# Kernel tuning notes

Hardware: AMD Instinct MI355X
Metric: run time of the kernel (lower is better)

The kernel has to match this reference:

```python
import jax, jax.numpy as jnp
import numpy as np

N = 8192
NFEAT = 512
NHID = 256
NCLASS = 40
EDGE_P = 0.002  # ~16 avg degree


def setup_inputs() -> dict:
    key = jax.random.key(0)
    k1, k2, k3, k4 = jax.random.split(key, 4)
    x = jax.random.normal(k1, (N, NFEAT), dtype=jnp.float32)
    # unnormalized binary adjacency without self loops (module adds eye itself)
    adj = (jax.random.uniform(k2, (N, N)) < EDGE_P).astype(jnp.float32)
    # GCNConv weights: torch.rand(in, out) -> uniform[0,1)
    W1 = jax.random.uniform(k3, (NFEAT, NHID), dtype=jnp.float32)
    W2 = jax.random.uniform(k4, (NHID, NCLASS), dtype=jnp.float32)
    return {"x": x, "adj": adj, "W1": W1, "W2": W2}


def reference(x, adj, W1, W2):
    n = adj.shape[0]
    # add self loops: in_adj.to_dense() + eye
    A_hat = adj + jnp.eye(n, dtype=adj.dtype)
    # normalize_adj: D^{-1/2} A_hat D^{-1/2} (diag matmuls == row/col scaling)
    d = A_hat.sum(-1) ** -0.5  # [N]
    norm_adj = d[:, None] * A_hat * d[None, :]
    # conv1: relu(adj @ x @ W1); dropout is identity in eval mode
    h = jax.nn.relu((norm_adj @ x) @ W1)
    # conv2 reuses the same normalized adjacency (only one DGG layer by default)
    h2 = jax.nn.relu((norm_adj @ h) @ W2)
    return jax.nn.log_softmax(h2, axis=-1)
```

## Files before the change

kernel.cpp:

```cpp
#include <hip/hip_runtime.h>
#include <math.h>

#define NV 8192
#define CAP 64

typedef __attribute__((ext_vector_type(8))) short short8;
typedef __attribute__((ext_vector_type(4))) float f32x4;

static __device__ __forceinline__ unsigned short f2bf(float v) {
  unsigned int u = __float_as_uint(v);
  unsigned int r = (u + 0x7fffu + ((u >> 16) & 1u)) >> 16;
  return (unsigned short)r;
}
static __device__ __forceinline__ float bf2f(unsigned short h) {
  return __uint_as_float(((unsigned int)h) << 16);
}

__global__ __launch_bounds__(256) void build_graph(
    const float* __restrict__ adj, int* __restrict__ cols,
    int* __restrict__ rowcount, float* __restrict__ dinv,
    float* __restrict__ diagv) {
  int row = blockIdx.x;
  int t = threadIdx.x;
  int lane = t & 63;
  __shared__ int cnt;
  __shared__ int diag_nz;
  __shared__ int wsum[4];
  if (t == 0) { cnt = 0; diag_nz = 0; }
  __syncthreads();
  const float4* arow = (const float4*)(adj + (size_t)row * NV);
  int mycount = 0;
  for (int i = t; i < NV / 4; i += 256) {
    float4 v = arow[i];
    float va[4] = {v.x, v.y, v.z, v.w};
#pragma unroll
    for (int j = 0; j < 4; j++) {
      bool nz = (va[j] != 0.0f);
      mycount += nz ? 1 : 0;
      int c = i * 4 + j;
      bool isdiag = nz && (c == row);
      bool take = nz && !isdiag;
      if (isdiag) diag_nz = 1;
      unsigned long long m = __ballot(take);
      if (m != 0ull) {
        int tot = __popcll(m);
        int pre = __popcll(m & ((1ull << lane) - 1ull));
        int leader = __ffsll((unsigned long long)m) - 1;
        int base = 0;
        if (lane == leader) base = atomicAdd(&cnt, tot);
        base = __shfl(base, leader, 64);
        if (take) {
          int p = base + pre;
          if (p < CAP) cols[(size_t)row * CAP + p] = c;
        }
      }
    }
  }
  for (int off = 32; off > 0; off >>= 1) mycount += __shfl_xor(mycount, off, 64);
  if (lane == 0) wsum[t >> 6] = mycount;
  __syncthreads();
  if (t == 0) {
    int nnz = wsum[0] + wsum[1] + wsum[2] + wsum[3];
    float deg = (float)nnz + 1.0f;
    dinv[row] = 1.0f / sqrtf(deg);
    diagv[row] = diag_nz ? 2.0f : 1.0f;
    rowcount[row] = cnt > CAP ? CAP : cnt;
  }
}

__global__ __launch_bounds__(256) void split_a(
    const float* __restrict__ x, unsigned short* __restrict__ Ah,
    unsigned short* __restrict__ Al) {
  int i = blockIdx.x * 256 + threadIdx.x;
  float4 v = ((const float4*)x)[i];
  ushort4 h, l;
  h.x = f2bf(v.x); l.x = f2bf(v.x - bf2f(h.x));
  h.y = f2bf(v.y); l.y = f2bf(v.y - bf2f(h.y));
  h.z = f2bf(v.z); l.z = f2bf(v.z - bf2f(h.z));
  h.w = f2bf(v.w); l.w = f2bf(v.w - bf2f(h.w));
  ((ushort4*)Ah)[i] = h;
  ((ushort4*)Al)[i] = l;
}

__global__ __launch_bounds__(256) void split_w1t(
    const float* __restrict__ W1, unsigned short* __restrict__ Bh,
    unsigned short* __restrict__ Bl) {
  int n = blockIdx.x;
  int k = blockIdx.y * 256 + threadIdx.x;
  float v = W1[(size_t)k * 256 + n];
  unsigned short h = f2bf(v);
  Bh[(size_t)n * 512 + k] = h;
  Bl[(size_t)n * 512 + k] = f2bf(v - bf2f(h));
}

__global__ __launch_bounds__(256) void gemm1_mfma(
    const unsigned short* __restrict__ Ah, const unsigned short* __restrict__ Al,
    const unsigned short* __restrict__ Bh, const unsigned short* __restrict__ Bl,
    float* __restrict__ C) {
  const int K = 512;
  __shared__ __align__(16) unsigned short sAh[128][40];
  __shared__ __align__(16) unsigned short sAl[128][40];
  __shared__ __align__(16) unsigned short sBh[64][40];
  __shared__ __align__(16) unsigned short sBl[64][40];
  int t = threadIdx.x;
  int bn = blockIdx.x * 64;
  int bm = blockIdx.y * 128;
  int lane = t & 63, w = t >> 6;
  int quad = lane >> 4, m16 = lane & 15;
  f32x4 acc[2][4] = {};
  for (int k0 = 0; k0 < K; k0 += 32) {
#pragma unroll
    for (int i = 0; i < 2; i++) {
      int id = t + i * 256;
      int row = id >> 2, q = id & 3;
      *(uint4*)&sAh[row][q * 8] = *(const uint4*)&Ah[(size_t)(bm + row) * K + k0 + q * 8];
      *(uint4*)&sAl[row][q * 8] = *(const uint4*)&Al[(size_t)(bm + row) * K + k0 + q * 8];
    }
    {
      int row = t >> 2, q = t & 3;
      *(uint4*)&sBh[row][q * 8] = *(const uint4*)&Bh[(size_t)(bn + row) * K + k0 + q * 8];
      *(uint4*)&sBl[row][q * 8] = *(const uint4*)&Bl[(size_t)(bn + row) * K + k0 + q * 8];
    }
    __syncthreads();
    short8 ah[2], al[2], bh[4], bl[4];
#pragma unroll
    for (int i = 0; i < 2; i++) {
      ah[i] = *(const short8*)&sAh[w * 32 + i * 16 + m16][quad * 8];
      al[i] = *(const short8*)&sAl[w * 32 + i * 16 + m16][quad * 8];
    }
#pragma unroll
    for (int j = 0; j < 4; j++) {
      bh[j] = *(const short8*)&sBh[j * 16 + m16][quad * 8];
      bl[j] = *(const short8*)&sBl[j * 16 + m16][quad * 8];
    }
#pragma unroll
    for (int i = 0; i < 2; i++)
#pragma unroll
      for (int j = 0; j < 4; j++) {
        acc[i][j] = __builtin_amdgcn_mfma_f32_16x16x32_bf16(ah[i], bh[j], acc[i][j], 0, 0, 0);
        acc[i][j] = __builtin_amdgcn_mfma_f32_16x16x32_bf16(al[i], bh[j], acc[i][j], 0, 0, 0);
        acc[i][j] = __builtin_amdgcn_mfma_f32_16x16x32_bf16(ah[i], bl[j], acc[i][j], 0, 0, 0);
      }
    __syncthreads();
  }
#pragma unroll
  for (int i = 0; i < 2; i++)
#pragma unroll
    for (int j = 0; j < 4; j++)
#pragma unroll
      for (int r = 0; r < 4; r++)
        C[(size_t)(bm + w * 32 + i * 16 + quad * 4 + r) * 256 + bn + j * 16 + m16] =
            acc[i][j][r];
}

__global__ __launch_bounds__(256) void gemm_f32(
    const float* __restrict__ A, const float* __restrict__ B,
    float* __restrict__ C, int M, int K, int Nvalid, int ldb, int ldc) {
  __shared__ float As[16][68];
  __shared__ float Bs[16][64];
  int t = threadIdx.x;
  int bm0 = blockIdx.y * 64;
  int bn0 = blockIdx.x * 64;
  int tx = t & 15, ty = t >> 4;
  int ar = t >> 2;
  int ak = (t & 3) * 4;
  int bk = t >> 4;
  int bn = (t & 15) * 4;
  float acc[4][4] = {};
  for (int k0 = 0; k0 < K; k0 += 16) {
    float4 av = *(const float4*)(A + (size_t)(bm0 + ar) * K + k0 + ak);
    float4 bv;
    int bc = bn0 + bn;
    if (bc + 3 < Nvalid) {
      bv = *(const float4*)(B + (size_t)(k0 + bk) * ldb + bc);
    } else {
      bv.x = (bc + 0 < Nvalid) ? B[(size_t)(k0 + bk) * ldb + bc + 0] : 0.0f;
      bv.y = (bc + 1 < Nvalid) ? B[(size_t)(k0 + bk) * ldb + bc + 1] : 0.0f;
      bv.z = (bc + 2 < Nvalid) ? B[(size_t)(k0 + bk) * ldb + bc + 2] : 0.0f;
      bv.w = (bc + 3 < Nvalid) ? B[(size_t)(k0 + bk) * ldb + bc + 3] : 0.0f;
    }
    As[ak + 0][ar] = av.x;
    As[ak + 1][ar] = av.y;
    As[ak + 2][ar] = av.z;
    As[ak + 3][ar] = av.w;
    *(float4*)(&Bs[bk][bn]) = bv;
    __syncthreads();
#pragma unroll
    for (int kk = 0; kk < 16; kk++) {
      float4 a = *(const float4*)(&As[kk][ty * 4]);
      float4 b = *(const float4*)(&Bs[kk][tx * 4]);
      acc[0][0] += a.x * b.x; acc[0][1] += a.x * b.y; acc[0][2] += a.x * b.z; acc[0][3] += a.x * b.w;
      acc[1][0] += a.y * b.x; acc[1][1] += a.y * b.y; acc[1][2] += a.y * b.z; acc[1][3] += a.y * b.w;
      acc[2][0] += a.z * b.x; acc[2][1] += a.z * b.y; acc[2][2] += a.z * b.z; acc[2][3] += a.z * b.w;
      acc[3][0] += a.w * b.x; acc[3][1] += a.w * b.y; acc[3][2] += a.w * b.z; acc[3][3] += a.w * b.w;
    }
    __syncthreads();
  }
#pragma unroll
  for (int i = 0; i < 4; i++) {
    *(float4*)(C + (size_t)(bm0 + ty * 4 + i) * ldc + bn0 + tx * 4) =
        make_float4(acc[i][0], acc[i][1], acc[i][2], acc[i][3]);
  }
}

__global__ __launch_bounds__(256) void spmm_relu_k(
    const float* __restrict__ Z, const int* __restrict__ cols,
    const int* __restrict__ rowcount, const float* __restrict__ dinv,
    const float* __restrict__ diagv, float* __restrict__ H) {
  int lane = threadIdx.x & 63;
  int row = blockIdx.x * 4 + (threadIdx.x >> 6);
  const float4* Zr = (const float4*)Z;
  float di = dinv[row];
  float4 z = Zr[(size_t)row * 64 + lane];
  float dd = diagv[row] * di;
  float4 acc;
  acc.x = dd * z.x; acc.y = dd * z.y; acc.z = dd * z.z; acc.w = dd * z.w;
  int cnt = rowcount[row];
  const int* cr = cols + (size_t)row * CAP;
  int e = 0;
  for (; e + 4 <= cnt; e += 4) {
    int c0 = cr[e + 0], c1 = cr[e + 1], c2 = cr[e + 2], c3 = cr[e + 3];
    float w0 = dinv[c0], w1 = dinv[c1], w2 = dinv[c2], w3 = dinv[c3];
    float4 g0 = Zr[(size_t)c0 * 64 + lane];
    float4 g1 = Zr[(size_t)c1 * 64 + lane];
    float4 g2 = Zr[(size_t)c2 * 64 + lane];
    float4 g3 = Zr[(size_t)c3 * 64 + lane];
    acc.x += w0 * g0.x + w1 * g1.x + w2 * g2.x + w3 * g3.x;
    acc.y += w0 * g0.y + w1 * g1.y + w2 * g2.y + w3 * g3.y;
    acc.z += w0 * g0.z + w1 * g1.z + w2 * g2.z + w3 * g3.z;
    acc.w += w0 * g0.w + w1 * g1.w + w2 * g2.w + w3 * g3.w;
  }
  for (; e < cnt; e++) {
    int c = cr[e];
    float w = dinv[c];
    float4 g = Zr[(size_t)c * 64 + lane];
    acc.x += w * g.x; acc.y += w * g.y; acc.z += w * g.z; acc.w += w * g.w;
  }
  float4 o;
  o.x = fmaxf(acc.x * di, 0.0f);
  o.y = fmaxf(acc.y * di, 0.0f);
  o.z = fmaxf(acc.z * di, 0.0f);
  o.w = fmaxf(acc.w * di, 0.0f);
  ((float4*)H)[(size_t)row * 64 + lane] = o;
}

__global__ __launch_bounds__(256) void spmm2_lsm_k(
    const float* __restrict__ Z, const int* __restrict__ cols,
    const int* __restrict__ rowcount, const float* __restrict__ dinv,
    const float* __restrict__ diagv, float* __restrict__ out) {
  int lane = threadIdx.x & 63;
  int row = blockIdx.x * 4 + (threadIdx.x >> 6);
  float di = dinv[row];
  float acc = diagv[row] * di * Z[(size_t)row * 64 + lane];
  int cnt = rowcount[row];
  const int* cr = cols + (size_t)row * CAP;
  int e = 0;
  for (; e + 4 <= cnt; e += 4) {
    int c0 = cr[e + 0], c1 = cr[e + 1], c2 = cr[e + 2], c3 = cr[e + 3];
    float w0 = dinv[c0], w1 = dinv[c1], w2 = dinv[c2], w3 = dinv[c3];
    acc += w0 * Z[(size_t)c0 * 64 + lane] + w1 * Z[(size_t)c1 * 64 + lane] +
           w2 * Z[(size_t)c2 * 64 + lane] + w3 * Z[(size_t)c3 * 64 + lane];
  }
  for (; e < cnt; e++) {
    int c = cr[e];
    acc += dinv[c] * Z[(size_t)c * 64 + lane];
  }
  float h2 = (lane < 40) ? fmaxf(acc * di, 0.0f) : -INFINITY;
  float m = h2;
  for (int off = 32; off > 0; off >>= 1) m = fmaxf(m, __shfl_xor(m, off, 64));
  float ex = (lane < 40) ? expf(h2 - m) : 0.0f;
  float s = ex;
  for (int off = 32; off > 0; off >>= 1) s += __shfl_xor(s, off, 64);
  float ls = logf(s);
  if (lane < 40) out[(size_t)row * 40 + lane] = h2 - m - ls;
}

extern "C" void kernel_launch(void* const* d_in, const int* in_sizes, int n_in,
                              void* d_out, int out_size, void* d_ws, size_t ws_size,
                              hipStream_t stream) {
  (void)in_sizes; (void)n_in; (void)out_size; (void)ws_size;
  const float* x   = (const float*)d_in[0];
  const float* adj = (const float*)d_in[1];
  const float* W1  = (const float*)d_in[2];
  const float* W2  = (const float*)d_in[3];
  float* out = (float*)d_out;
  char* ws = (char*)d_ws;

  int*   cols     = (int*)(ws);
  int*   rowcount = (int*)(ws + 2097152);
  float* dinv     = (float*)(ws + 2129920);
  float* diagv    = (float*)(ws + 2162688);
  float* XW1      = (float*)(ws + 2195456);
  float* H        = (float*)(ws + 10584064);
  float* HW2      = (float*)(ws + 18972672);
  unsigned short* Ah = (unsigned short*)(ws + 21069824);
  unsigned short* Al = (unsigned short*)(ws + 29458432);
  unsigned short* Bh = (unsigned short*)(ws + 37847040);
  unsigned short* Bl = (unsigned short*)(ws + 38109184);

  hipLaunchKernelGGL(build_graph, dim3(NV), dim3(256), 0, stream,
                     adj, cols, rowcount, dinv, diagv);
  hipLaunchKernelGGL(split_a, dim3(NV * 512 / 4 / 256), dim3(256), 0, stream,
                     x, Ah, Al);
  hipLaunchKernelGGL(split_w1t, dim3(256, 2), dim3(256), 0, stream,
                     W1, Bh, Bl);
  hipLaunchKernelGGL(gemm1_mfma, dim3(4, 64), dim3(256), 0, stream,
                     Ah, Al, Bh, Bl, XW1);
  hipLaunchKernelGGL(spmm_relu_k, dim3(NV / 4), dim3(256), 0, stream,
                     XW1, cols, rowcount, dinv, diagv, H);
  hipLaunchKernelGGL(gemm_f32, dim3(1, 128), dim3(256), 0, stream,
                     H, W2, HW2, NV, 256, 40, 40, 64);
  hipLaunchKernelGGL(spmm2_lsm_k, dim3(NV / 4), dim3(256), 0, stream,
                     HW2, cols, rowcount, dinv, diagv, out);
}
```

Baseline: 437.9 us.

## Fuse bf16 split into GEMM1 and co-launch with graph build

Merges the graph-building kernel, the x and W1 bf16 hi/lo split kernels, and the MFMA GEMM into one launch. The first 256 blocks do the GEMM, converting fp32 inputs to split bf16 on the fly in shared memory. The remaining blocks scan adjacency rows. This removes intermediate bf16 buffers and extra launches, and lets the compute-bound GEMM overlap the bandwidth-bound adjacency scan. In exchange, each GEMM tile redoes the conversions and transposes W1 through scalar shared-memory stores.

```diff
diff --git a/kernel.cpp b/kernel.cpp
--- a/kernel.cpp
+++ b/kernel.cpp
@@ -16,141 +16,132 @@
   return __uint_as_float(((unsigned int)h) << 16);
 }
 
-__global__ __launch_bounds__(256) void build_graph(
-    const float* __restrict__ adj, int* __restrict__ cols,
+__global__ __launch_bounds__(256) void mega_build_gemm1(
+    const float* __restrict__ adj, const float* __restrict__ x,
+    const float* __restrict__ W1, int* __restrict__ cols,
     int* __restrict__ rowcount, float* __restrict__ dinv,
-    float* __restrict__ diagv) {
-  int row = blockIdx.x;
-  int t = threadIdx.x;
-  int lane = t & 63;
-  __shared__ int cnt;
-  __shared__ int diag_nz;
-  __shared__ int wsum[4];
-  if (t == 0) { cnt = 0; diag_nz = 0; }
-  __syncthreads();
-  const float4* arow = (const float4*)(adj + (size_t)row * NV);
-  int mycount = 0;
-  for (int i = t; i < NV / 4; i += 256) {
-    float4 v = arow[i];
-    float va[4] = {v.x, v.y, v.z, v.w};
-#pragma unroll
-    for (int j = 0; j < 4; j++) {
-      bool nz = (va[j] != 0.0f);
-      mycount += nz ? 1 : 0;
-      int c = i * 4 + j;
-      bool isdiag = nz && (c == row);
-      bool take = nz && !isdiag;
-      if (isdiag) diag_nz = 1;
-      unsigned long long m = __ballot(take);
-      if (m != 0ull) {
-        int tot = __popcll(m);
-        int pre = __popcll(m & ((1ull << lane) - 1ull));
-        int leader = __ffsll((unsigned long long)m) - 1;
-        int base = 0;
-        if (lane == leader) base = atomicAdd(&cnt, tot);
-        base = __shfl(base, leader, 64);
-        if (take) {
-          int p = base + pre;
-          if (p < CAP) cols[(size_t)row * CAP + p] = c;
-        }
-      }
-    }
-  }
-  for (int off = 32; off > 0; off >>= 1) mycount += __shfl_xor(mycount, off, 64);
-  if (lane == 0) wsum[t >> 6] = mycount;
-  __syncthreads();
-  if (t == 0) {
-    int nnz = wsum[0] + wsum[1] + wsum[2] + wsum[3];
-    float deg = (float)nnz + 1.0f;
-    dinv[row] = 1.0f / sqrtf(deg);
-    diagv[row] = diag_nz ? 2.0f : 1.0f;
-    rowcount[row] = cnt > CAP ? CAP : cnt;
-  }
-}
-
-__global__ __launch_bounds__(256) void split_a(
-    const float* __restrict__ x, unsigned short* __restrict__ Ah,
-    unsigned short* __restrict__ Al) {
-  int i = blockIdx.x * 256 + threadIdx.x;
-  float4 v = ((const float4*)x)[i];
-  ushort4 h, l;
-  h.x = f2bf(v.x); l.x = f2bf(v.x - bf2f(h.x));
-  h.y = f2bf(v.y); l.y = f2bf(v.y - bf2f(h.y));
-  h.z = f2bf(v.z); l.z = f2bf(v.z - bf2f(h.z));
-  h.w = f2bf(v.w); l.w = f2bf(v.w - bf2f(h.w));
-  ((ushort4*)Ah)[i] = h;
-  ((ushort4*)Al)[i] = l;
-}
-
-__global__ __launch_bounds__(256) void split_w1t(
-    const float* __restrict__ W1, unsigned short* __restrict__ Bh,
-    unsigned short* __restrict__ Bl) {
-  int n = blockIdx.x;
-  int k = blockIdx.y * 256 + threadIdx.x;
-  float v = W1[(size_t)k * 256 + n];
-  unsigned short h = f2bf(v);
-  Bh[(size_t)n * 512 + k] = h;
-  Bl[(size_t)n * 512 + k] = f2bf(v - bf2f(h));
-}
-
-__global__ __launch_bounds__(256) void gemm1_mfma(
-    const unsigned short* __restrict__ Ah, const unsigned short* __restrict__ Al,
-    const unsigned short* __restrict__ Bh, const unsigned short* __restrict__ Bl,
-    float* __restrict__ C) {
-  const int K = 512;
+    float* __restrict__ diagv, float* __restrict__ XW1) {
   __shared__ __align__(16) unsigned short sAh[128][40];
   __shared__ __align__(16) unsigned short sAl[128][40];
   __shared__ __align__(16) unsigned short sBh[64][40];
   __shared__ __align__(16) unsigned short sBl[64][40];
+  __shared__ int cnt;
+  __shared__ int diag_nz;
+  __shared__ int wsum[4];
+
   int t = threadIdx.x;
-  int bn = blockIdx.x * 64;
-  int bm = blockIdx.y * 128;
-  int lane = t & 63, w = t >> 6;
-  int quad = lane >> 4, m16 = lane & 15;
-  f32x4 acc[2][4] = {};
-  for (int k0 = 0; k0 < K; k0 += 32) {
-#pragma unroll
-    for (int i = 0; i < 2; i++) {
-      int id = t + i * 256;
-      int row = id >> 2, q = id & 3;
-      *(uint4*)&sAh[row][q * 8] = *(const uint4*)&Ah[(size_t)(bm + row) * K + k0 + q * 8];
-      *(uint4*)&sAl[row][q * 8] = *(const uint4*)&Al[(size_t)(bm + row) * K + k0 + q * 8];
-    }
-    {
-      int row = t >> 2, q = t & 3;
-      *(uint4*)&sBh[row][q * 8] = *(const uint4*)&Bh[(size_t)(bn + row) * K + k0 + q * 8];
-      *(uint4*)&sBl[row][q * 8] = *(const uint4*)&Bl[(size_t)(bn + row) * K + k0 + q * 8];
-    }
-    __syncthreads();
-    short8 ah[2], al[2], bh[4], bl[4];
-#pragma unroll
-    for (int i = 0; i < 2; i++) {
-      ah[i] = *(const short8*)&sAh[w * 32 + i * 16 + m16][quad * 8];
-      al[i] = *(const short8*)&sAl[w * 32 + i * 16 + m16][quad * 8];
-    }
-#pragma unroll
-    for (int j = 0; j < 4; j++) {
-      bh[j] = *(const short8*)&sBh[j * 16 + m16][quad * 8];
-      bl[j] = *(const short8*)&sBl[j * 16 + m16][quad * 8];
+  int lane = t & 63;
+
+  if (blockIdx.x < 256) {
+    const int K = 512;
+    int b = blockIdx.x;
+    int bn = (b & 3) * 64;
+    int bm = (b >> 2) * 128;
+    int w = t >> 6;
+    int quad = lane >> 4, m16 = lane & 15;
+    f32x4 acc[2][4] = {};
+    for (int k0 = 0; k0 < K; k0 += 32) {
+#pragma unroll
+      for (int i = 0; i < 4; i++) {
+        int id = t + i * 256;
+        int row = id >> 3;
+        int fq = id & 7;
+        float4 v = *(const float4*)&x[(size_t)(bm + row) * K + k0 + fq * 4];
+        ushort4 h, l;
+        h.x = f2bf(v.x); l.x = f2bf(v.x - bf2f(h.x));
+        h.y = f2bf(v.y); l.y = f2bf(v.y - bf2f(h.y));
+        h.z = f2bf(v.z); l.z = f2bf(v.z - bf2f(h.z));
+        h.w = f2bf(v.w); l.w = f2bf(v.w - bf2f(h.w));
+        *(ushort4*)&sAh[row][fq * 4] = h;
+        *(ushort4*)&sAl[row][fq * 4] = l;
+      }
+#pragma unroll
+      for (int j = 0; j < 2; j++) {
+        int id = t + j * 256;
+        int k = id >> 4;
+        int n4 = (id & 15) * 4;
+        float4 v = *(const float4*)&W1[(size_t)(k0 + k) * 256 + bn + n4];
+        float va[4] = {v.x, v.y, v.z, v.w};
+#pragma unroll
+        for (int c = 0; c < 4; c++) {
+          unsigned short h = f2bf(va[c]);
+          sBh[n4 + c][k] = h;
+          sBl[n4 + c][k] = f2bf(va[c] - bf2f(h));
+        }
+      }
+      __syncthreads();
+      short8 ah[2], al[2], bh[4], bl[4];
+#pragma unroll
+      for (int i = 0; i < 2; i++) {
+        ah[i] = *(const short8*)&sAh[w * 32 + i * 16 + m16][quad * 8];
+        al[i] = *(const short8*)&sAl[w * 32 + i * 16 + m16][quad * 8];
+      }
+#pragma unroll
+      for (int j = 0; j < 4; j++) {
+        bh[j] = *(const short8*)&sBh[j * 16 + m16][quad * 8];
+        bl[j] = *(const short8*)&sBl[j * 16 + m16][quad * 8];
+      }
+#pragma unroll
+      for (int i = 0; i < 2; i++)
+#pragma unroll
+        for (int j = 0; j < 4; j++) {
+          acc[i][j] = __builtin_amdgcn_mfma_f32_16x16x32_bf16(ah[i], bh[j], acc[i][j], 0, 0, 0);
+          acc[i][j] = __builtin_amdgcn_mfma_f32_16x16x32_bf16(al[i], bh[j], acc[i][j], 0, 0, 0);
+          acc[i][j] = __builtin_amdgcn_mfma_f32_16x16x32_bf16(ah[i], bl[j], acc[i][j], 0, 0, 0);
+        }
+      __syncthreads();
     }
 #pragma unroll
     for (int i = 0; i < 2; i++)
 #pragma unroll
+      for (int j = 0; j < 4; j++)
+#pragma unroll
+        for (int r = 0; r < 4; r++)
+          XW1[(size_t)(bm + w * 32 + i * 16 + quad * 4 + r) * 256 + bn + j * 16 + m16] =
+              acc[i][j][r];
+  } else {
+    int row = blockIdx.x - 256;
+    if (t == 0) { cnt = 0; diag_nz = 0; }
+    __syncthreads();
+    const float4* arow = (const float4*)(adj + (size_t)row * NV);
+    int mycount = 0;
+    for (int i = t; i < NV / 4; i += 256) {
+      float4 v = arow[i];
+      float va[4] = {v.x, v.y, v.z, v.w};
+#pragma unroll
       for (int j = 0; j < 4; j++) {
-        acc[i][j] = __builtin_amdgcn_mfma_f32_16x16x32_bf16(ah[i], bh[j], acc[i][j], 0, 0, 0);
-        acc[i][j] = __builtin_amdgcn_mfma_f32_16x16x32_bf16(al[i], bh[j], acc[i][j], 0, 0, 0);
-        acc[i][j] = __builtin_amdgcn_mfma_f32_16x16x32_bf16(ah[i], bl[j], acc[i][j], 0, 0, 0);
-      }
-    __syncthreads();
-  }
-#pragma unroll
-  for (int i = 0; i < 2; i++)
-#pragma unroll
-    for (int j = 0; j < 4; j++)
-#pragma unroll
-      for (int r = 0; r < 4; r++)
-        C[(size_t)(bm + w * 32 + i * 16 + quad * 4 + r) * 256 + bn + j * 16 + m16] =
-            acc[i][j][r];
+        bool nz = (va[j] != 0.0f);
+        mycount += nz ? 1 : 0;
+        int c = i * 4 + j;
+        bool isdiag = nz && (c == row);
+        bool take = nz && !isdiag;
+        if (isdiag) diag_nz = 1;
+        unsigned long long m = __ballot(take);
+        if (m != 0ull) {
+          int tot = __popcll(m);
+          int pre = __popcll(m & ((1ull << lane) - 1ull));
+          int leader = __ffsll((unsigned long long)m) - 1;
+          int base = 0;
+          if (lane == leader) base = atomicAdd(&cnt, tot);
+          base = __shfl(base, leader, 64);
+          if (take) {
+            int p = base + pre;
+            if (p < CAP) cols[(size_t)row * CAP + p] = c;
+          }
+        }
+      }
+    }
+    for (int off = 32; off > 0; off >>= 1) mycount += __shfl_xor(mycount, off, 64);
+    if (lane == 0) wsum[t >> 6] = mycount;
+    __syncthreads();
+    if (t == 0) {
+      int nnz = wsum[0] + wsum[1] + wsum[2] + wsum[3];
+      float deg = (float)nnz + 1.0f;
+      dinv[row] = 1.0f / sqrtf(deg);
+      diagv[row] = diag_nz ? 2.0f : 1.0f;
+      rowcount[row] = cnt > CAP ? CAP : cnt;
+    }
+  }
 }
 
 __global__ __launch_bounds__(256) void gemm_f32(
@@ -293,19 +284,9 @@
   float* XW1      = (float*)(ws + 2195456);
   float* H        = (float*)(ws + 10584064);
   float* HW2      = (float*)(ws + 18972672);
-  unsigned short* Ah = (unsigned short*)(ws + 21069824);
-  unsigned short* Al = (unsigned short*)(ws + 29458432);
-  unsigned short* Bh = (unsigned short*)(ws + 37847040);
-  unsigned short* Bl = (unsigned short*)(ws + 38109184);
-
-  hipLaunchKernelGGL(build_graph, dim3(NV), dim3(256), 0, stream,
-                     adj, cols, rowcount, dinv, diagv);
-  hipLaunchKernelGGL(split_a, dim3(NV * 512 / 4 / 256), dim3(256), 0, stream,
-                     x, Ah, Al);
-  hipLaunchKernelGGL(split_w1t, dim3(256, 2), dim3(256), 0, stream,
-                     W1, Bh, Bl);
-  hipLaunchKernelGGL(gemm1_mfma, dim3(4, 64), dim3(256), 0, stream,
-                     Ah, Al, Bh, Bl, XW1);
+
+  hipLaunchKernelGGL(mega_build_gemm1, dim3(256 + NV), dim3(256), 0, stream,
+                     adj, x, W1, cols, rowcount, dinv, diagv, XW1);
   hipLaunchKernelGGL(spmm_relu_k, dim3(NV / 4), dim3(256), 0, stream,
                      XW1, cols, rowcount, dinv, diagv, H);
   hipLaunchKernelGGL(gemm_f32, dim3(1, 128), dim3(256), 0, stream,
```

After: 434.0 us. Within noise of the previous version (-0.9%).
